# Kernel optimization log

Measured on AMD Instinct MI355X. Metric: run time of the kernel, lower is better.

The kernel has to match this reference:

```python
import jax, jax.numpy as jnp
import numpy as np

T, B, C, H = 2048, 2, 1024, 16
D = C // H
SCALE = D ** -0.5
WSTD = C ** -0.5  # keep activations O(1) so softmax is not saturated


def setup_inputs() -> dict:
    key = jax.random.key(0)
    ks = jax.random.split(key, 6)
    return {
        "x": jax.random.normal(ks[0], (T, B, C), dtype=jnp.float32),
        "wq": jax.random.normal(ks[1], (C, C), dtype=jnp.float32) * WSTD,
        "wk": jax.random.normal(ks[2], (C, C), dtype=jnp.float32) * WSTD,
        "wv": jax.random.normal(ks[3], (C, C), dtype=jnp.float32) * WSTD,
        "wo": jax.random.normal(ks[4], (C, C), dtype=jnp.float32) * WSTD,
        "bo": jax.random.normal(ks[5], (C,), dtype=jnp.float32) * 0.02,
    }


def reference(x, wq, wk, wv, wo, bo):
    t, b, c = x.shape
    x2 = x.reshape(t * b, c)
    # SelfAttentionLinears: q scaled by head_dim^-0.5 inside the addmm
    q = (x2 @ wq) * SCALE
    k = x2 @ wk
    v = x2 @ wv
    # fairseq layout: (T, B*H, D) -> (B*H, T, D)
    q = q.reshape(t, b * H, D).transpose(1, 0, 2)
    k = k.reshape(t, b * H, D).transpose(1, 0, 2)
    v = v.reshape(t, b * H, D).transpose(1, 0, 2)
    # strided_bmm1: scores [B*H, T, T]
    scores = jnp.einsum('bqd,bkd->bqk', q, k)
    attn = jax.nn.softmax(scores, axis=-1)
    # strided_bmm2: context [B*H, T, D]
    ctx = jnp.einsum('bqk,bkd->bqd', attn, v)
    out = ctx.transpose(1, 0, 2).reshape(t, b, c)
    return out @ wo + bo
```

## Files before the change

kernel.cpp:

```cpp
#include <hip/hip_runtime.h>
#include <math.h>

#define T_DIM 2048
#define B_DIM 2
#define C_DIM 1024
#define H_DIM 16
#define D_DIM 64
#define M_DIM (T_DIM * B_DIM)
#define SCALE_QL2 0.18033688f

typedef short short8  __attribute__((ext_vector_type(8)));
typedef float f32x4   __attribute__((ext_vector_type(4)));
typedef float f32x16  __attribute__((ext_vector_type(16)));
typedef unsigned short ushort_t;

#if __has_builtin(__builtin_amdgcn_exp2f)
#define EXP2(x) __builtin_amdgcn_exp2f(x)
#else
#define EXP2(x) exp2f(x)
#endif

__device__ __forceinline__ unsigned short f2bf(float f) {
    unsigned int u = __builtin_bit_cast(unsigned int, f);
    u += 0x7FFFu + ((u >> 16) & 1u);
    return (unsigned short)(u >> 16);
}

__device__ __forceinline__ void gl_lds16(const void* g, void* l) {
    __builtin_amdgcn_global_load_lds(
        (const __attribute__((address_space(1))) void*)g,
        (__attribute__((address_space(3))) void*)l, 16, 0, 0);
}

__global__ __launch_bounds__(256) void prep(
    const float* __restrict__ x,
    const float* __restrict__ wq, const float* __restrict__ wk,
    const float* __restrict__ wv, const float* __restrict__ wo,
    ushort_t* __restrict__ xb,
    ushort_t* __restrict__ wqkv_t, ushort_t* __restrict__ wo_t)
{
    __shared__ float tile[64][65];
    const int tid = threadIdx.x;
    const int z   = blockIdx.z;

    if (z == 4) {
        const size_t base =
            ((size_t)(blockIdx.y * 16 + blockIdx.x)) * 16384 + (size_t)tid * 8;
#pragma unroll
        for (int j = 0; j < 8; ++j) {
            const size_t i = base + (size_t)j * 2048;
            const float4 v0 = *(const float4*)&x[i];
            const float4 v1 = *(const float4*)&x[i + 4];
            ushort_t o[8] = {f2bf(v0.x), f2bf(v0.y), f2bf(v0.z), f2bf(v0.w),
                             f2bf(v1.x), f2bf(v1.y), f2bf(v1.z), f2bf(v1.w)};
            *(uint4*)&xb[i] = *(uint4*)o;
        }
        return;
    }

    const int k0 = blockIdx.x * 64;
    const int n0 = blockIdx.y * 64;
    const float* src = (z == 0) ? wq : (z == 1) ? wk : (z == 2) ? wv : wo;
    ushort_t* dst = (z < 3) ? (wqkv_t + (size_t)z * C_DIM * C_DIM) : wo_t;

    const int r = tid >> 4;
    const int c = (tid & 15) * 4;
#pragma unroll
    for (int i = 0; i < 4; ++i) {
        const float4 v = *(const float4*)&src[(size_t)(k0 + r + i * 16) * C_DIM + n0 + c];
        *(float4*)&tile[r + i * 16][c] = v;
    }
    __syncthreads();
#pragma unroll
    for (int i = 0; i < 4; ++i) {
        const int r2 = r + i * 16;
        ushort4 o;
        o.x = f2bf(tile[c + 0][r2]); o.y = f2bf(tile[c + 1][r2]);
        o.z = f2bf(tile[c + 2][r2]); o.w = f2bf(tile[c + 3][r2]);
        *(ushort4*)&dst[(size_t)(n0 + r2) * C_DIM + k0 + c] = o;
    }
}

__global__ __launch_bounds__(256) void qkv_mfma(
    const ushort_t* __restrict__ xb, const ushort_t* __restrict__ wt,
    ushort_t* __restrict__ q_ws, ushort_t* __restrict__ k_ws,
    ushort_t* __restrict__ v_ws)
{
    __shared__ ushort_t lds[18432];
    ushort_t* As = lds;
    ushort_t* Bs = lds + 4096;

    const int tid  = threadIdx.x;
    const int n0   = blockIdx.x * 128;
    const int m0   = blockIdx.y * 128;
    const int w    = tid >> 6;
    const int lane = tid & 63;
    const int l16  = lane & 15;
    const int quad = lane >> 4;
    const int wm   = (w >> 1) * 64;
    const int wn   = (w & 1) * 64;

    const int o0 = tid * 8, o1 = o0 + 2048;
    const ushort_t* a0 = xb + (size_t)(m0 + (o0 >> 5)) * C_DIM + (o0 & 31);
    const ushort_t* a1 = xb + (size_t)(m0 + (o1 >> 5)) * C_DIM + (o1 & 31);
    const ushort_t* b0 = wt + (size_t)(n0 + (o0 >> 5)) * C_DIM + (o0 & 31);
    const ushort_t* b1 = wt + (size_t)(n0 + (o1 >> 5)) * C_DIM + (o1 & 31);

    f32x4 acc[4][4] = {};

    for (int k0 = 0; k0 < C_DIM; k0 += 32) {
        __syncthreads();
        gl_lds16(a0 + k0, As + o0);
        gl_lds16(a1 + k0, As + o1);
        gl_lds16(b0 + k0, Bs + o0);
        gl_lds16(b1 + k0, Bs + o1);
        __syncthreads();

        short8 af[4], bf[4];
#pragma unroll
        for (int mi = 0; mi < 4; ++mi)
            af[mi] = *(const short8*)&As[(wm + mi * 16 + l16) * 32 + quad * 8];
#pragma unroll
        for (int ni = 0; ni < 4; ++ni)
            bf[ni] = *(const short8*)&Bs[(wn + ni * 16 + l16) * 32 + quad * 8];
#pragma unroll
        for (int mi = 0; mi < 4; ++mi)
#pragma unroll
            for (int ni = 0; ni < 4; ++ni)
                acc[mi][ni] = __builtin_amdgcn_mfma_f32_16x16x32_bf16(
                    af[mi], bf[ni], acc[mi][ni], 0, 0, 0);
    }

    __syncthreads();
    ushort_t* Ep = lds + w * 4608;

    const int mat = n0 >> 10;
    const int cb  = (n0 & 1023) + wn;
    const int h   = cb >> 6;
    ushort_t* dst = (mat == 0) ? q_ws : (mat == 1) ? k_ws : v_ws;
    const float sc = (mat == 0) ? SCALE_QL2 : 1.0f;

#pragma unroll
    for (int mi = 0; mi < 4; ++mi)
#pragma unroll
        for (int ni = 0; ni < 4; ++ni)
#pragma unroll
            for (int r = 0; r < 4; ++r)
                Ep[(mi * 16 + quad * 4 + r) * 72 + ni * 16 + l16] =
                    f2bf(acc[mi][ni][r] * sc);

    const int rq = lane >> 3;
    const int c8 = (lane & 7) * 8;
#pragma unroll
    for (int p = 0; p < 8; ++p) {
        const int row = p * 8 + rq;
        const uint4 val = *(const uint4*)&Ep[row * 72 + c8];
        const int m = m0 + wm + row;
        const int t = m >> 1, b = m & 1;
        *(uint4*)&dst[((size_t)(b * H_DIM + h) * T_DIM + t) * D_DIM + c8] = val;
    }
}

__global__ __launch_bounds__(256) void v_transpose(
    const ushort_t* __restrict__ vn, ushort_t* __restrict__ vt)
{
    __shared__ ushort_t tile[64][72];
    const int tid = threadIdx.x;
    const int t0  = blockIdx.x * 64;
    const int bh  = blockIdx.y;
    const int r   = tid >> 3;
    const int c   = (tid & 7) * 8;
#pragma unroll
    for (int i = 0; i < 2; ++i)
        *(uint4*)&tile[r + i * 32][c] =
            *(const uint4*)&vn[((size_t)bh * T_DIM + t0 + r + i * 32) * D_DIM + c];
    __syncthreads();
#pragma unroll
    for (int i = 0; i < 2; ++i) {
        const int rd = r + i * 32;
        ushort_t o[8];
#pragma unroll
        for (int j = 0; j < 8; ++j) o[j] = tile[c + j][rd];
        *(uint4*)&vt[((size_t)bh * D_DIM + rd) * T_DIM + t0 + c] = *(uint4*)o;
    }
}

__global__ __launch_bounds__(256) void attn_mfma(
    const ushort_t* __restrict__ q, const ushort_t* __restrict__ k,
    const ushort_t* __restrict__ v, ushort_t* __restrict__ ctx)
{
    __shared__ ushort_t Ks [64][72];
    __shared__ ushort_t Vts[64][72];

    const int tid  = threadIdx.x;
    const int bh   = blockIdx.x;
    const int q0   = blockIdx.y * 128;
    const int w    = tid >> 6;
    const int lane = tid & 63;
    const int l32  = lane & 31;
    const int hi   = lane >> 5;

    const int r0 = tid >> 3,         c80 = (tid & 7) * 8;
    const int r1 = r0 + 32;
    const ushort_t* kbase = k + (size_t)bh * T_DIM * D_DIM;
    const ushort_t* vbase = v + (size_t)bh * D_DIM * T_DIM;

    short8 qreg[4];
    {
        const ushort_t* qrow =
            q + ((size_t)bh * T_DIM + q0 + 32 * w + l32) * D_DIM + hi * 8;
#pragma unroll
        for (int s = 0; s < 4; ++s)
            qreg[s] = *(const short8*)(qrow + s * 16);
    }

    short8 vones;
#pragma unroll
    for (int j = 0; j < 8; ++j) vones[j] = (short)0x3F80;

    f32x16 O0 = {}, O1 = {};
    f32x16 Osum = {};

    const ushort_t* kp0 = kbase + (size_t)r0 * D_DIM + c80;
    const ushort_t* kp1 = kbase + (size_t)r1 * D_DIM + c80;
    const ushort_t* vp0 = vbase + (size_t)r0 * T_DIM + c80;
    const ushort_t* vp1 = vbase + (size_t)r1 * T_DIM + c80;
    uint4 kr0 = *(const uint4*)kp0;  kp0 += 64 * D_DIM;
    uint4 kr1 = *(const uint4*)kp1;  kp1 += 64 * D_DIM;
    uint4 vr0 = *(const uint4*)vp0;  vp0 += 64;
    uint4 vr1 = *(const uint4*)vp1;  vp1 += 64;

    for (int kt = 0; kt < 32; ++kt) {
        __syncthreads();
        *(uint4*)&Ks[r0][c80]  = kr0;
        *(uint4*)&Ks[r1][c80]  = kr1;
        *(uint4*)&Vts[r0][c80] = vr0;
        *(uint4*)&Vts[r1][c80] = vr1;
        if (kt + 1 < 32) {
            kr0 = *(const uint4*)kp0;  kp0 += 64 * D_DIM;
            kr1 = *(const uint4*)kp1;  kp1 += 64 * D_DIM;
            vr0 = *(const uint4*)vp0;  vp0 += 64;
            vr1 = *(const uint4*)vp1;  vp1 += 64;
        }
        __syncthreads();

        f32x16 st0 = {}, st1 = {};
        __builtin_amdgcn_s_setprio(1);
#pragma unroll
        for (int s = 0; s < 4; ++s) {
            const short8 ak0 = *(const short8*)&Ks[l32]     [s * 16 + hi * 8];
            const short8 ak1 = *(const short8*)&Ks[32 + l32][s * 16 + hi * 8];
            st0 = __builtin_amdgcn_mfma_f32_32x32x16_bf16(ak0, qreg[s], st0, 0, 0, 0);
            st1 = __builtin_amdgcn_mfma_f32_32x32x16_bf16(ak1, qreg[s], st1, 0, 0, 0);
        }
        __builtin_amdgcn_s_setprio(0);

        unsigned wpk0[8], wpk1[8];
#pragma unroll
        for (int i = 0; i < 8; ++i) {
            const float a0 = EXP2(st0[2 * i]);
            const float a1 = EXP2(st0[2 * i + 1]);
            const float b0 = EXP2(st1[2 * i]);
            const float b1 = EXP2(st1[2 * i + 1]);
            wpk0[i] = __builtin_amdgcn_perm(
                __builtin_bit_cast(unsigned, a1),
                __builtin_bit_cast(unsigned, a0), 0x07060302u);
            wpk1[i] = __builtin_amdgcn_perm(
                __builtin_bit_cast(unsigned, b1),
                __builtin_bit_cast(unsigned, b0), 0x07060302u);
        }

        short8 ap[4];
#pragma unroll
        for (int pr = 0; pr < 2; ++pr) {
            unsigned x0 = wpk0[4 * pr + 0], y0 = wpk0[4 * pr + 2];
            unsigned x1 = wpk0[4 * pr + 1], y1 = wpk0[4 * pr + 3];
            asm("v_permlane32_swap_b32 %0, %1" : "+v"(x0), "+v"(y0));
            asm("v_permlane32_swap_b32 %0, %1" : "+v"(x1), "+v"(y1));
            uint4 fw = {x0, x1, y0, y1};
            ap[pr] = __builtin_bit_cast(short8, fw);

            unsigned u0 = wpk1[4 * pr + 0], z0 = wpk1[4 * pr + 2];
            unsigned u1 = wpk1[4 * pr + 1], z1 = wpk1[4 * pr + 3];
            asm("v_permlane32_swap_b32 %0, %1" : "+v"(u0), "+v"(z0));
            asm("v_permlane32_swap_b32 %0, %1" : "+v"(u1), "+v"(z1));
            uint4 fw1 = {u0, u1, z0, z1};
            ap[2 + pr] = __builtin_bit_cast(short8, fw1);
        }

        __builtin_amdgcn_s_setprio(1);
#pragma unroll
        for (int s = 0; s < 4; ++s) {
            Osum = __builtin_amdgcn_mfma_f32_32x32x16_bf16(ap[s], vones, Osum, 0, 0, 0);
            const short8 bv0 = *(const short8*)&Vts[l32]     [s * 16 + hi * 8];
            const short8 bv1 = *(const short8*)&Vts[32 + l32][s * 16 + hi * 8];
            O0 = __builtin_amdgcn_mfma_f32_32x32x16_bf16(ap[s], bv0, O0, 0, 0, 0);
            O1 = __builtin_amdgcn_mfma_f32_32x32x16_bf16(ap[s], bv1, O1, 0, 0, 0);
        }
        __builtin_amdgcn_s_setprio(0);
    }

    const int b = bh >> 4;
    const int h = bh & 15;
#pragma unroll
    for (int reg = 0; reg < 16; ++reg) {
        const int qrel = (reg & 3) + 8 * (reg >> 2) + 4 * hi;
        const float inv = 1.0f / Osum[reg];
        const int row = q0 + 32 * w + qrel;
        const size_t base = ((size_t)row * B_DIM + b) * C_DIM + h * 64 + l32;
        ctx[base]      = f2bf(O0[reg] * inv);
        ctx[base + 32] = f2bf(O1[reg] * inv);
    }
}

__global__ __launch_bounds__(256) void out_mfma(
    const ushort_t* __restrict__ ctx, const ushort_t* __restrict__ wot,
    const float* __restrict__ bo, float* __restrict__ out)
{
    __shared__ ushort_t As[128 * 32];
    __shared__ ushort_t Bs[64 * 32];

    const int tid  = threadIdx.x;
    const int n0   = blockIdx.x * 64;
    const int m0   = blockIdx.y * 128;
    const int w    = tid >> 6;
    const int lane = tid & 63;
    const int l16  = lane & 15;
    const int quad = lane >> 4;
    const int wm   = (w >> 1) * 64;
    const int wn   = (w & 1) * 32;

    const int o0 = tid * 8, o1 = o0 + 2048;
    const ushort_t* a0 = ctx + (size_t)(m0 + (o0 >> 5)) * C_DIM + (o0 & 31);
    const ushort_t* a1 = ctx + (size_t)(m0 + (o1 >> 5)) * C_DIM + (o1 & 31);
    const ushort_t* b0 = wot + (size_t)(n0 + (o0 >> 5)) * C_DIM + (o0 & 31);

    f32x4 acc[4][2] = {};

    for (int k0 = 0; k0 < C_DIM; k0 += 32) {
        __syncthreads();
        gl_lds16(a0 + k0, As + o0);
        gl_lds16(a1 + k0, As + o1);
        gl_lds16(b0 + k0, Bs + o0);
        __syncthreads();

        short8 af[4], bf[2];
#pragma unroll
        for (int mi = 0; mi < 4; ++mi)
            af[mi] = *(const short8*)&As[(wm + mi * 16 + l16) * 32 + quad * 8];
#pragma unroll
        for (int ni = 0; ni < 2; ++ni)
            bf[ni] = *(const short8*)&Bs[(wn + ni * 16 + l16) * 32 + quad * 8];
#pragma unroll
        for (int mi = 0; mi < 4; ++mi)
#pragma unroll
            for (int ni = 0; ni < 2; ++ni)
                acc[mi][ni] = __builtin_amdgcn_mfma_f32_16x16x32_bf16(
                    af[mi], bf[ni], acc[mi][ni], 0, 0, 0);
    }

#pragma unroll
    for (int ni = 0; ni < 2; ++ni) {
        const int n = n0 + wn + ni * 16 + l16;
        const float bias = bo[n];
#pragma unroll
        for (int mi = 0; mi < 4; ++mi) {
            const int mb = m0 + wm + mi * 16 + quad * 4;
#pragma unroll
            for (int r = 0; r < 4; ++r)
                out[(size_t)(mb + r) * C_DIM + n] = acc[mi][ni][r] + bias;
        }
    }
}

extern "C" void kernel_launch(void* const* d_in, const int* in_sizes, int n_in,
                              void* d_out, int out_size, void* d_ws, size_t ws_size,
                              hipStream_t stream)
{
    const float* x  = (const float*)d_in[0];
    const float* wq = (const float*)d_in[1];
    const float* wk = (const float*)d_in[2];
    const float* wv = (const float*)d_in[3];
    const float* wo = (const float*)d_in[4];
    const float* bo = (const float*)d_in[5];
    float* out = (float*)d_out;

    const size_t CC  = (size_t)C_DIM * C_DIM;
    const size_t MC  = (size_t)M_DIM * C_DIM;
    ushort_t* xb     = (ushort_t*)d_ws;
    ushort_t* wqkv_t = xb + MC;
    ushort_t* wo_t   = wqkv_t + 3 * CC;
    ushort_t* q_ws   = wo_t + CC;
    ushort_t* k_ws   = q_ws + MC;
    ushort_t* v_nat  = k_ws + MC;
    ushort_t* v_t    = v_nat + MC;
    ushort_t* ctx    = v_t + MC;

    hipLaunchKernelGGL(prep, dim3(16, 16, 5), dim3(256), 0, stream,
                       x, wq, wk, wv, wo, xb, wqkv_t, wo_t);
    hipLaunchKernelGGL(qkv_mfma, dim3(24, 32), dim3(256), 0, stream,
                       xb, wqkv_t, q_ws, k_ws, v_nat);
    hipLaunchKernelGGL(v_transpose, dim3(32, 32), dim3(256), 0, stream,
                       v_nat, v_t);
    hipLaunchKernelGGL(attn_mfma, dim3(32, 16), dim3(256), 0, stream,
                       q_ws, k_ws, v_t, ctx);
    hipLaunchKernelGGL(out_mfma, dim3(16, 32), dim3(256), 0, stream,
                       ctx, wo_t, bo, out);
}
```

Measured before the change: 189.4 us.

## Fuse V transpose into QKV epilogue and halve attention block size

The QKV GEMM epilogue now writes V directly in the transposed [B*H, D, T] layout through an LDS staging tile, so the separate v_transpose kernel and its extra global round trip are gone. The attention kernel now uses 128-thread blocks covering 64 query rows, launched on a 32x32 grid with a launch_bounds hint of 4 blocks per CU, which doubles the block count. Each thread now loads four K/V rows per tile instead of two. The trade-off is that each K/V tile is now reused by fewer query rows, so K/V global and LDS traffic per query goes up, while more blocks are available to hide latency.

```diff
diff --git a/kernel.cpp b/kernel.cpp
--- a/kernel.cpp
+++ b/kernel.cpp
@@ -84,7 +84,7 @@
 __global__ __launch_bounds__(256) void qkv_mfma(
     const ushort_t* __restrict__ xb, const ushort_t* __restrict__ wt,
     ushort_t* __restrict__ q_ws, ushort_t* __restrict__ k_ws,
-    ushort_t* __restrict__ v_ws)
+    ushort_t* __restrict__ v_ws )
 {
     __shared__ ushort_t lds[18432];
     ushort_t* As = lds;
@@ -137,7 +137,33 @@
     const int mat = n0 >> 10;
     const int cb  = (n0 & 1023) + wn;
     const int h   = cb >> 6;
-    ushort_t* dst = (mat == 0) ? q_ws : (mat == 1) ? k_ws : v_ws;
+    const int rq  = lane >> 3;
+    const int c8  = (lane & 7) * 8;
+
+    if (mat == 2) {
+#pragma unroll
+        for (int mi = 0; mi < 4; ++mi)
+#pragma unroll
+            for (int ni = 0; ni < 4; ++ni)
+#pragma unroll
+                for (int r = 0; r < 4; ++r) {
+                    const int mrel = mi * 16 + quad * 4 + r;
+                    Ep[(ni * 16 + l16) * 72 + (mrel >> 1) + ((mrel & 1) << 5)] =
+                        f2bf(acc[mi][ni][r]);
+                }
+        const int T0 = (m0 + wm) >> 1;
+        const int b  = c8 >> 5;
+        const int tr = c8 & 31;
+#pragma unroll
+        for (int p = 0; p < 8; ++p) {
+            const int d = p * 8 + rq;
+            const uint4 val = *(const uint4*)&Ep[d * 72 + c8];
+            *(uint4*)&v_ws[((size_t)(b * H_DIM + h) * D_DIM + d) * T_DIM + T0 + tr] = val;
+        }
+        return;
+    }
+
+    ushort_t* dst = (mat == 0) ? q_ws : k_ws;
     const float sc = (mat == 0) ? SCALE_QL2 : 1.0f;
 
 #pragma unroll
@@ -149,8 +175,6 @@
                 Ep[(mi * 16 + quad * 4 + r) * 72 + ni * 16 + l16] =
                     f2bf(acc[mi][ni][r] * sc);
 
-    const int rq = lane >> 3;
-    const int c8 = (lane & 7) * 8;
 #pragma unroll
     for (int p = 0; p < 8; ++p) {
         const int row = p * 8 + rq;
@@ -161,31 +185,7 @@
     }
 }
 
-__global__ __launch_bounds__(256) void v_transpose(
-    const ushort_t* __restrict__ vn, ushort_t* __restrict__ vt)
-{
-    __shared__ ushort_t tile[64][72];
-    const int tid = threadIdx.x;
-    const int t0  = blockIdx.x * 64;
-    const int bh  = blockIdx.y;
-    const int r   = tid >> 3;
-    const int c   = (tid & 7) * 8;
-#pragma unroll
-    for (int i = 0; i < 2; ++i)
-        *(uint4*)&tile[r + i * 32][c] =
-            *(const uint4*)&vn[((size_t)bh * T_DIM + t0 + r + i * 32) * D_DIM + c];
-    __syncthreads();
-#pragma unroll
-    for (int i = 0; i < 2; ++i) {
-        const int rd = r + i * 32;
-        ushort_t o[8];
-#pragma unroll
-        for (int j = 0; j < 8; ++j) o[j] = tile[c + j][rd];
-        *(uint4*)&vt[((size_t)bh * D_DIM + rd) * T_DIM + t0 + c] = *(uint4*)o;
-    }
-}
-
-__global__ __launch_bounds__(256) void attn_mfma(
+__global__ __launch_bounds__(128, 4) void attn_mfma(
     const ushort_t* __restrict__ q, const ushort_t* __restrict__ k,
     const ushort_t* __restrict__ v, ushort_t* __restrict__ ctx)
 {
@@ -194,14 +194,14 @@
 
     const int tid  = threadIdx.x;
     const int bh   = blockIdx.x;
-    const int q0   = blockIdx.y * 128;
+    const int q0   = blockIdx.y * 64;
     const int w    = tid >> 6;
     const int lane = tid & 63;
     const int l32  = lane & 31;
     const int hi   = lane >> 5;
 
-    const int r0 = tid >> 3,         c80 = (tid & 7) * 8;
-    const int r1 = r0 + 32;
+    const int r0  = tid >> 3;
+    const int c80 = (tid & 7) * 8;
     const ushort_t* kbase = k + (size_t)bh * T_DIM * D_DIM;
     const ushort_t* vbase = v + (size_t)bh * D_DIM * T_DIM;
 
@@ -221,26 +221,30 @@
     f32x16 O0 = {}, O1 = {};
     f32x16 Osum = {};
 
-    const ushort_t* kp0 = kbase + (size_t)r0 * D_DIM + c80;
-    const ushort_t* kp1 = kbase + (size_t)r1 * D_DIM + c80;
-    const ushort_t* vp0 = vbase + (size_t)r0 * T_DIM + c80;
-    const ushort_t* vp1 = vbase + (size_t)r1 * T_DIM + c80;
-    uint4 kr0 = *(const uint4*)kp0;  kp0 += 64 * D_DIM;
-    uint4 kr1 = *(const uint4*)kp1;  kp1 += 64 * D_DIM;
-    uint4 vr0 = *(const uint4*)vp0;  vp0 += 64;
-    uint4 vr1 = *(const uint4*)vp1;  vp1 += 64;
+    const ushort_t* kp = kbase + (size_t)r0 * D_DIM + c80;
+    const ushort_t* vp = vbase + (size_t)r0 * T_DIM + c80;
+    uint4 kr[4], vr[4];
+#pragma unroll
+    for (int i = 0; i < 4; ++i) {
+        kr[i] = *(const uint4*)(kp + i * 16 * D_DIM);
+        vr[i] = *(const uint4*)(vp + i * 16 * T_DIM);
+    }
+    kp += 64 * D_DIM;  vp += 64;
 
     for (int kt = 0; kt < 32; ++kt) {
         __syncthreads();
-        *(uint4*)&Ks[r0][c80]  = kr0;
-        *(uint4*)&Ks[r1][c80]  = kr1;
-        *(uint4*)&Vts[r0][c80] = vr0;
-        *(uint4*)&Vts[r1][c80] = vr1;
+#pragma unroll
+        for (int i = 0; i < 4; ++i) {
+            *(uint4*)&Ks [r0 + 16 * i][c80] = kr[i];
+            *(uint4*)&Vts[r0 + 16 * i][c80] = vr[i];
+        }
         if (kt + 1 < 32) {
-            kr0 = *(const uint4*)kp0;  kp0 += 64 * D_DIM;
-            kr1 = *(const uint4*)kp1;  kp1 += 64 * D_DIM;
-            vr0 = *(const uint4*)vp0;  vp0 += 64;
-            vr1 = *(const uint4*)vp1;  vp1 += 64;
+#pragma unroll
+            for (int i = 0; i < 4; ++i) {
+                kr[i] = *(const uint4*)(kp + i * 16 * D_DIM);
+                vr[i] = *(const uint4*)(vp + i * 16 * T_DIM);
+            }
+            kp += 64 * D_DIM;  vp += 64;
         }
         __syncthreads();
 
@@ -392,17 +396,14 @@
     ushort_t* wo_t   = wqkv_t + 3 * CC;
     ushort_t* q_ws   = wo_t + CC;
     ushort_t* k_ws   = q_ws + MC;
-    ushort_t* v_nat  = k_ws + MC;
-    ushort_t* v_t    = v_nat + MC;
+    ushort_t* v_t    = k_ws + MC;
     ushort_t* ctx    = v_t + MC;
 
     hipLaunchKernelGGL(prep, dim3(16, 16, 5), dim3(256), 0, stream,
                        x, wq, wk, wv, wo, xb, wqkv_t, wo_t);
     hipLaunchKernelGGL(qkv_mfma, dim3(24, 32), dim3(256), 0, stream,
-                       xb, wqkv_t, q_ws, k_ws, v_nat);
-    hipLaunchKernelGGL(v_transpose, dim3(32, 32), dim3(256), 0, stream,
-                       v_nat, v_t);
-    hipLaunchKernelGGL(attn_mfma, dim3(32, 16), dim3(256), 0, stream,
+                       xb, wqkv_t, q_ws, k_ws, v_t);
+    hipLaunchKernelGGL(attn_mfma, dim3(32, 32), dim3(128), 0, stream,
                        q_ws, k_ws, v_t, ctx);
     hipLaunchKernelGGL(out_mfma, dim3(16, 32), dim3(256), 0, stream,
                        ctx, wo_t, bo, out);
```

After: 309.6 us. 63.5% more time.
